# Kernel optimization log

Measured on AMD Instinct MI355X. Metric: run time of the kernel, lower is better.

Reference implementation:

```python
import jax, jax.numpy as jnp
import numpy as np
import math

H = 128          # num_heads
DN = 128         # qk_nope_head_dim
DR = 64          # qk_rope_head_dim
DV = 128         # v_head_dim
RQ = 1536        # q_lora_rank
RKV = 512        # kv_lora_rank
HSZ = 5120       # hidden_size
EPS = 1e-6


def rms_norm(x, w, eps=EPS):
    var = jnp.mean(x * x, axis=-1, keepdims=True)
    return x * jax.lax.rsqrt(var + eps) * w


def rope(x):
    # x: [b, h, s, d] ; standard NeoX-style rotary, base 10000, positions 0..s-1
    d = x.shape[-1]
    s = x.shape[-2]
    inv_freq = 1.0 / (10000.0 ** (jnp.arange(0, d, 2, dtype=jnp.float32) / d))  # [d/2]
    t = jnp.arange(s, dtype=jnp.float32)
    freqs = jnp.outer(t, inv_freq)                      # [s, d/2]
    cos = jnp.concatenate([jnp.cos(freqs)] * 2, -1)     # [s, d]
    sin = jnp.concatenate([jnp.sin(freqs)] * 2, -1)
    x1, x2 = jnp.split(x, 2, axis=-1)
    rot = jnp.concatenate([-x2, x1], axis=-1)
    return (x * cos + rot * sin).astype(x.dtype)


def setup_inputs() -> dict:
    key = jax.random.key(0)
    ks = jax.random.split(key, 8)
    std = 0.02
    hidden_states = jax.random.normal(ks[0], (1, 1024, HSZ), dtype=jnp.float32)
    # weights stored [in, out] (transposed vs torch nn.Linear)
    Wq_c = jax.random.normal(ks[1], (HSZ, RQ), dtype=jnp.float32) * std
    q_norm_w = jnp.ones((RQ,), dtype=jnp.float32)
    Wq_d = jax.random.normal(ks[2], (RQ, H * (DN + DR)), dtype=jnp.float32) * std
    Wkv_c = jax.random.normal(ks[3], (HSZ, RKV + DR), dtype=jnp.float32) * std
    kv_norm_w = jnp.ones((RKV,), dtype=jnp.float32)
    Wkv_d = jax.random.normal(ks[4], (RKV, H * (DN + DV)), dtype=jnp.float32) * std
    Wo = jax.random.normal(ks[5], (H * DV, HSZ), dtype=jnp.float32) * std
    return {"hidden_states": hidden_states, "Wq_c": Wq_c, "q_norm_w": q_norm_w,
            "Wq_d": Wq_d, "Wkv_c": Wkv_c, "kv_norm_w": kv_norm_w,
            "Wkv_d": Wkv_d, "Wo": Wo}


def reference(hidden_states, Wq_c, q_norm_w, Wq_d, Wkv_c, kv_norm_w, Wkv_d, Wo):
    B, S, _ = hidden_states.shape
    # --- Query: compress -> RMSNorm -> decompress ---
    q = rms_norm(hidden_states @ Wq_c, q_norm_w) @ Wq_d          # [B,S,H*(DN+DR)]
    q = q.reshape(B, S, H, DN + DR).transpose(0, 2, 1, 3)        # [B,H,S,DN+DR]
    q_nope, q_rope = q[..., :DN], q[..., DN:]
    # --- KV: compress (this is the compressed_kv_cache) ---
    compress_kv_full = hidden_states @ Wkv_c                     # [B,S,RKV+DR]
    compressed_kv_cache = jax.lax.stop_gradient(compress_kv_full)
    compress_kv = compress_kv_full[..., :RKV]
    k_rope = compress_kv_full[..., RKV:][:, None, :, :]          # [B,1,S,DR]
    # --- KV decompress ---
    kv = rms_norm(compress_kv, kv_norm_w) @ Wkv_d                # [B,S,H*(DN+DV)]
    kv = kv.reshape(B, S, H, DN + DV).transpose(0, 2, 1, 3)      # [B,H,S,DN+DV]
    k_nope, v = kv[..., :DN], kv[..., DN:]
    # --- split RoPE on rope slices only ---
    q_rope = rope(q_rope)                                        # [B,H,S,DR]
    k_rope = rope(k_rope)                                        # [B,1,S,DR]
    # --- concat nope|rope (k_rope broadcasts over heads) ---
    qc = jnp.concatenate([q_nope, q_rope], axis=-1)              # [B,H,S,DN+DR]
    kc = jnp.concatenate([k_nope, jnp.broadcast_to(k_rope, (B, H, S, DR))], axis=-1)
    # --- attention ---
    scale = 1.0 / math.sqrt(DN + DR)
    scores = jnp.einsum('bhqd,bhkd->bhqk', qc, kc) * scale       # [B,H,S,S]
    probs = jax.nn.softmax(scores.astype(jnp.float32), axis=-1).astype(qc.dtype)
    out = jnp.einsum('bhqk,bhkd->bhqd', probs, v)                # [B,H,S,DV]
    out = out.transpose(0, 2, 1, 3).reshape(B, S, H * DV)
    out = out @ Wo                                               # [B,S,HSZ]
    return out, compressed_kv_cache
```

## Files before the change

### kernel.cpp

```cpp
#include <hip/hip_runtime.h>


typedef __attribute__((ext_vector_type(8))) short short8;
typedef __attribute__((ext_vector_type(4))) float f32x4;
typedef unsigned short u16;

__device__ __forceinline__ u16 f2bf(float f) {
  union { float f; unsigned u; } v; v.f = f;
  unsigned r = v.u + 0x7fffu + ((v.u >> 16) & 1u);
  return (u16)(r >> 16);
}
__device__ __forceinline__ float bf2f(u16 s) {
  union { unsigned u; float f; } v; v.u = ((unsigned)s) << 16; return v.f;
}

__device__ __forceinline__ void gl_lds16(const u16* g, u16* l) {
  __builtin_amdgcn_global_load_lds(
      (const __attribute__((address_space(1))) void*)g,
      (__attribute__((address_space(3))) void*)l,
      16, 0, 0);
}

#define BARX()  asm volatile("s_barrier" ::: "memory")
#define LGKM0() do { asm volatile("s_waitcnt lgkmcnt(0)" ::: "memory"); \
                     __builtin_amdgcn_sched_barrier(0); } while (0)
#define VMW(n)  asm volatile("s_waitcnt vmcnt(" #n ")" ::: "memory")

__global__ void k_zero(float* __restrict__ p, int n4) {
  int i = blockIdx.x * 256 + threadIdx.x;
  if (i < n4) ((float4*)p)[i] = make_float4(0.f, 0.f, 0.f, 0.f);
}

__global__ void k_cast(const float* __restrict__ in, u16* __restrict__ out, int n4) {
  int i = blockIdx.x * 256 + threadIdx.x;
  if (i < n4) {
    float4 v = ((const float4*)in)[i];
    ushort4 o;
    o.x = f2bf(v.x); o.y = f2bf(v.y); o.z = f2bf(v.z); o.w = f2bf(v.w);
    ((ushort4*)out)[i] = o;
  }
}

__global__ void k_wt(const float* __restrict__ W, u16* __restrict__ WT,
                     int K, int N) {
  __shared__ u16 t[32][33];
  int n0 = blockIdx.x * 32, k0 = blockIdx.y * 32;
  int tx = threadIdx.x, ty = threadIdx.y;
#pragma unroll
  for (int r = 0; r < 4; r++) {
    int kl = ty + r * 8, n = n0 + tx;
    float v = (n < N) ? W[(size_t)(k0 + kl) * N + n] : 0.f;
    t[kl][tx] = f2bf(v);
  }
  __syncthreads();
#pragma unroll
  for (int r = 0; r < 4; r++) {
    int nl = ty + r * 8;
    WT[(size_t)(n0 + nl) * K + k0 + tx] = t[tx][nl];
  }
}

template<int OUT_MODE>
__global__ __launch_bounds__(256) void k_gemm_bt(
    const u16* __restrict__ A, const u16* __restrict__ BT,
    void* __restrict__ Cv, int M, int N, int K, int kChunk)
{
  __shared__ u16 As[128 * 32];
  __shared__ u16 Bs[128 * 32];
  const int tid = threadIdx.x;
  const int wave = tid >> 6, lane = tid & 63;
  const int qd = lane >> 4, l = lane & 15;
  const int bn0 = blockIdx.x * 128, bm0 = blockIdx.y * 128;
  const int k0 = blockIdx.z * kChunk;
  const int wrow = (wave >> 1) * 64, wcol = (wave & 1) * 64;
  const f32x4 fzero = {0.f, 0.f, 0.f, 0.f};

  f32x4 acc[4][4];
#pragma unroll
  for (int i = 0; i < 4; i++)
#pragma unroll
    for (int j = 0; j < 4; j++) acc[i][j] = fzero;

  const int sm = wave * 16 + (lane >> 2);
  const int sc = (lane & 3) * 8;
  const u16* a0 = A  + (size_t)(bm0 + sm) * K + sc;
  const u16* a1 = A  + (size_t)(bm0 + 64 + sm) * K + sc;
  const u16* b0 = BT + (size_t)(bn0 + sm) * K + sc;
  const u16* b1 = BT + (size_t)(bn0 + 64 + sm) * K + sc;
  u16* aD0 = As + wave * 512;
  u16* aD1 = As + 2048 + wave * 512;
  u16* bD0 = Bs + wave * 512;
  u16* bD1 = Bs + 2048 + wave * 512;

  const int kEnd = k0 + kChunk;
  for (int kt = k0; kt < kEnd; kt += 32) {
    gl_lds16(a0 + kt, aD0);
    gl_lds16(a1 + kt, aD1);
    gl_lds16(b0 + kt, bD0);
    gl_lds16(b1 + kt, bD1);
    __syncthreads();

    short8 af[4], bfr[4];
#pragma unroll
    for (int i = 0; i < 4; i++) af[i]  = *(const short8*)&As[(wrow + i * 16 + l) * 32 + qd * 8];
#pragma unroll
    for (int j = 0; j < 4; j++) bfr[j] = *(const short8*)&Bs[(wcol + j * 16 + l) * 32 + qd * 8];
#pragma unroll
    for (int i = 0; i < 4; i++)
#pragma unroll
      for (int j = 0; j < 4; j++)
        acc[i][j] = __builtin_amdgcn_mfma_f32_16x16x32_bf16(af[i], bfr[j], acc[i][j], 0, 0, 0);
    __syncthreads();
  }

#pragma unroll
  for (int i = 0; i < 4; i++) {
    int r = bm0 + wrow + i * 16 + qd * 4;
#pragma unroll
    for (int j = 0; j < 4; j++) {
      int c = bn0 + wcol + j * 16 + l;
      if (c < N) {
#pragma unroll
        for (int reg = 0; reg < 4; ++reg) {
          if (OUT_MODE == 1)
            ((u16*)Cv)[(size_t)(r + reg) * N + c] = f2bf(acc[i][j][reg]);
          else if (OUT_MODE == 0)
            ((float*)Cv)[(size_t)(r + reg) * N + c] = acc[i][j][reg];
          else
            atomicAdd(&((float*)Cv)[(size_t)(r + reg) * N + c], acc[i][j][reg]);
        }
      }
    }
  }
}

template<int OUT_MODE>
__global__ __launch_bounds__(512, 2) void k_gemm256(
    const u16* __restrict__ A, const u16* __restrict__ BT, void* __restrict__ Cv,
    int M, int N, int K, int kChunk)
{
  __shared__ u16 As[2][16384];
  __shared__ u16 Bs[2][16384];
  const int tid = threadIdx.x;
  const int w = tid >> 6, lane = tid & 63;
  const int wm = w >> 2, wn = w & 3;
  const int qd = lane >> 4, l = lane & 15;

  const int gx = gridDim.x, gy = gridDim.y;
  const int nwg = gx * gy * gridDim.z;
  int lin = blockIdx.x + gx * (blockIdx.y + gy * blockIdx.z);
  int lin2 = (lin & 7) * (nwg >> 3) + (lin >> 3);
  const int bx = lin2 % gx;
  const int byz = lin2 / gx;
  const int bm0 = (byz % gy) * 256;
  const int bn0 = bx * 256;
  const int k0  = (byz / gy) * kChunk;
  const int kcap = K - k0;
  const int myChunk = (kcap < kChunk) ? kcap : kChunk;
  const int ntiles = myChunk >> 6;
  const int niter  = ntiles >> 1;

  f32x4 acc[8][4];
  const f32x4 fz = {0.f, 0.f, 0.f, 0.f};
#pragma unroll
  for (int i = 0; i < 8; i++)
#pragma unroll
    for (int j = 0; j < 4; j++) acc[i][j] = fz;

#define STG(matP, rb, tI, hf, dstB)                                           \
  {                                                                           \
    const int _kt = k0 + (tI) * 64;                                           \
    _Pragma("unroll")                                                         \
    for (int _L = 0; _L < 2; ++_L) {                                          \
      const int _ob = (hf) * 8192 + _L * 4096 + w * 512;    \
      const int _o  = _ob + lane * 8;                                         \
      const int _r  = _o >> 6;                                                \
      const int _c  = (_o & 63) ^ ((_r & 7) << 3);                            \
      gl_lds16((matP) + (size_t)((rb) + _r) * K + _kt + _c, (dstB) + _ob);    \
    }                                                                         \
  }

#define LDA4(buf, mh)                                                         \
  _Pragma("unroll")                                                           \
  for (int _i = 0; _i < 4; ++_i) {                                            \
    const int _row = wm * 128 + (mh) * 64 + _i * 16 + l;                      \
    const int _sw = (_row & 7) << 3;                                          \
    af[_i][0] = *(const short8*)&(buf)[_row * 64 + ((qd * 8) ^ _sw)];         \
    af[_i][1] = *(const short8*)&(buf)[_row * 64 + ((32 + qd * 8) ^ _sw)];    \
  }

#define LDB2(buf, nh, dst)                                                    \
  _Pragma("unroll")                                                           \
  for (int _j = 0; _j < 2; ++_j) {                                            \
    const int _row = wn * 64 + (nh) * 32 + _j * 16 + l;                       \
    const int _sw = (_row & 7) << 3;                                          \
    dst[_j][0] = *(const short8*)&(buf)[_row * 64 + ((qd * 8) ^ _sw)];        \
    dst[_j][1] = *(const short8*)&(buf)[_row * 64 + ((32 + qd * 8) ^ _sw)];   \
  }

#define MFQ(mh, nh, bsrc)                                                     \
  __builtin_amdgcn_s_setprio(1);                                              \
  _Pragma("unroll")                                                           \
  for (int _i = 0; _i < 4; ++_i)                                              \
    _Pragma("unroll")                                                         \
    for (int _j = 0; _j < 2; ++_j) {                                          \
      f32x4 _a = acc[(mh) * 4 + _i][(nh) * 2 + _j];                           \
      _a = __builtin_amdgcn_mfma_f32_16x16x32_bf16(af[_i][0], bsrc[_j][0], _a, 0, 0, 0); \
      _a = __builtin_amdgcn_mfma_f32_16x16x32_bf16(af[_i][1], bsrc[_j][1], _a, 0, 0, 0); \
      acc[(mh) * 4 + _i][(nh) * 2 + _j] = _a;                                 \
    }                                                                         \
  __builtin_amdgcn_s_setprio(0);

  STG(BT, bn0, 0, 0, Bs[0]); STG(BT, bn0, 0, 1, Bs[0]);
  STG(A,  bm0, 0, 0, As[0]); STG(A,  bm0, 0, 1, As[0]);
  STG(BT, bn0, 1, 0, Bs[1]); STG(BT, bn0, 1, 1, Bs[1]);
  STG(A,  bm0, 1, 0, As[1]);
  VMW(6);
  BARX();

  short8 af[4][2], bf0[2][2], bf1[2][2];
  for (int j = 0; j < niter; ++j) {
    int t2 = 2 * j + 2; if (t2 >= ntiles) t2 -= ntiles;
    int t3 = t2 + 1;

    LDA4(As[0], 0); LDB2(Bs[0], 0, bf0);
    STG(A, bm0, 2 * j + 1, 1, As[1]);
    BARX(); LGKM0();
    MFQ(0, 0, bf0);
    BARX();

    LDB2(Bs[0], 1, bf1);
    BARX(); LGKM0();
    MFQ(0, 1, bf1);
    BARX();

    LDA4(As[0], 1);
    STG(BT, bn0, t2, 0, Bs[0]); STG(BT, bn0, t2, 1, Bs[0]);
    BARX(); LGKM0();
    MFQ(1, 1, bf1);
    BARX();

    STG(A, bm0, t2, 0, As[0]);
    VMW(6);
    BARX(); LGKM0();
    MFQ(1, 0, bf0);
    BARX();

    LDA4(As[1], 0); LDB2(Bs[1], 0, bf0);
    STG(A, bm0, t2, 1, As[0]);
    BARX(); LGKM0();
    MFQ(0, 0, bf0);
    BARX();

    LDB2(Bs[1], 1, bf1);
    BARX(); LGKM0();
    MFQ(0, 1, bf1);
    BARX();

    LDA4(As[1], 1);
    STG(BT, bn0, t3, 0, Bs[1]); STG(BT, bn0, t3, 1, Bs[1]);
    BARX(); LGKM0();
    MFQ(1, 1, bf1);
    BARX();

    STG(A, bm0, t3, 0, As[1]);
    VMW(6);
    BARX(); LGKM0();
    MFQ(1, 0, bf0);
    BARX();
  }
  asm volatile("s_waitcnt vmcnt(0)" ::: "memory");

#undef STG
#undef LDA4
#undef LDB2
#undef MFQ

#pragma unroll
  for (int i = 0; i < 8; ++i) {
    int r = bm0 + wm * 128 + i * 16 + qd * 4;
#pragma unroll
    for (int jj = 0; jj < 4; ++jj) {
      int c = bn0 + wn * 64 + jj * 16 + l;
#pragma unroll
      for (int reg = 0; reg < 4; ++reg) {
        if (OUT_MODE == 1)
          ((u16*)Cv)[(size_t)(r + reg) * N + c] = f2bf(acc[i][jj][reg]);
        else
          atomicAdd(&((float*)Cv)[(size_t)(r + reg) * N + c], acc[i][jj][reg]);
      }
    }
  }
}

__global__ void k_rmsnorm(const float* __restrict__ in, int istride, int W,
                          const float* __restrict__ w, u16* __restrict__ out) {
  int row = blockIdx.x, tid = threadIdx.x;
  const float* x = in + (size_t)row * istride;
  float s = 0.f;
  for (int i = tid; i < W; i += 256) { float v = x[i]; s += v * v; }
#pragma unroll
  for (int o = 32; o; o >>= 1) s += __shfl_xor(s, o);
  __shared__ float red[4];
  if ((tid & 63) == 0) red[tid >> 6] = s;
  __syncthreads();
  float tot = red[0] + red[1] + red[2] + red[3];
  float sc = rsqrtf(tot / (float)W + 1e-6f);
  for (int i = tid; i < W; i += 256)
    out[(size_t)row * W + i] = f2bf(x[i] * sc * w[i]);
}

__global__ void k_rope_q(u16* __restrict__ q) {
  int idx = blockIdx.x * 256 + threadIdx.x;
  int s = idx >> 12, r = idx & 4095, h = r >> 5, i = r & 31;
  float inv = expf((float)i * (-logf(10000.f) / 32.f));
  float ang = (float)s * inv, sn, cs;
  sincosf(ang, &sn, &cs);
  u16* p1 = q + (size_t)s * 24576 + h * 192 + 128 + i;
  u16* p2 = p1 + 32;
  float x1 = bf2f(*p1), x2 = bf2f(*p2);
  *p1 = f2bf(x1 * cs - x2 * sn);
  *p2 = f2bf(x2 * cs + x1 * sn);
}

__global__ void k_rope_k(const float* __restrict__ ckv, u16* __restrict__ kr) {
  int idx = blockIdx.x * 256 + threadIdx.x;
  int s = idx >> 5, i = idx & 31;
  float inv = expf((float)i * (-logf(10000.f) / 32.f));
  float ang = (float)s * inv, sn, cs;
  sincosf(ang, &sn, &cs);
  const float* src = ckv + (size_t)s * 576 + 512;
  float x1 = src[i], x2 = src[i + 32];
  kr[s * 64 + i]      = f2bf(x1 * cs - x2 * sn);
  kr[s * 64 + 32 + i] = f2bf(x2 * cs + x1 * sn);
}

__global__ void k_transpose_v(const u16* __restrict__ kv, u16* __restrict__ vt) {
  __shared__ u16 tile[32][33];
  int h = blockIdx.z, s0 = blockIdx.x * 32, d0 = blockIdx.y * 32;
  int tx = threadIdx.x, ty = threadIdx.y;
#pragma unroll
  for (int k2 = 0; k2 < 4; k2++) {
    int r = ty + k2 * 8;
    tile[r][tx] = kv[(size_t)(s0 + r) * 32768 + h * 256 + 128 + d0 + tx];
  }
  __syncthreads();
#pragma unroll
  for (int k2 = 0; k2 < 4; k2++) {
    int r = ty + k2 * 8;
    vt[(size_t)h * 131072 + (size_t)(d0 + r) * 1024 + s0 + tx] = tile[tx][r];
  }
}

__global__ __launch_bounds__(256, 2) void k_attn(
    const u16* __restrict__ q,
    const u16* __restrict__ kvn,
    const u16* __restrict__ kr,
    const u16* __restrict__ vt,
    u16* __restrict__ o)
{
  __shared__ u16 Ks[64][200];
  __shared__ u16 Vs[128][72];
  __shared__ u16 Ps[4][16][64];
  const int h = blockIdx.x, q0 = blockIdx.y * 64;
  const int tid = threadIdx.x, wave = tid >> 6, lane = tid & 63;
  const int qd = lane >> 4, l = lane & 15;
  const float scale = 0.07216878364870323f;
  const f32x4 fzero = {0.f, 0.f, 0.f, 0.f};

  short8 qf[6];
  {
    const u16* qp = q + (size_t)(q0 + wave * 16 + l) * 24576 + h * 192 + qd * 8;
#pragma unroll
    for (int kk = 0; kk < 6; kk++) qf[kk] = *(const short8*)(qp + kk * 32);
  }

  f32x4 Of[8];
#pragma unroll
  for (int jt = 0; jt < 8; jt++) Of[jt] = fzero;
  float m_i[4] = {-1e30f, -1e30f, -1e30f, -1e30f};
  float l_i[4] = {0.f, 0.f, 0.f, 0.f};

  for (int kt = 0; kt < 16; ++kt) {
    const int kv0 = kt * 64;
    __syncthreads();
#pragma unroll
    for (int it = 0; it < 6; ++it) {
      int ci = it * 256 + tid;
      int r = ci / 24, c = ci % 24;
      int col0 = c * 8;
      const u16* src = (col0 < 128)
          ? kvn + (size_t)(kv0 + r) * 32768 + h * 256 + col0
          : kr + (size_t)(kv0 + r) * 64 + (col0 - 128);
      *(short8*)&Ks[r][col0] = *(const short8*)src;
    }
#pragma unroll
    for (int it = 0; it < 4; ++it) {
      int ci = it * 256 + tid;
      int dv = ci >> 3, c = ci & 7;
      *(short8*)&Vs[dv][c * 8] =
          *(const short8*)(vt + (size_t)h * 131072 + (size_t)dv * 1024 + kv0 + c * 8);
    }
    __syncthreads();

    f32x4 sf[4];
#pragma unroll
    for (int j = 0; j < 4; j++) sf[j] = fzero;
#pragma unroll
    for (int kk = 0; kk < 6; kk++)
#pragma unroll
      for (int j = 0; j < 4; j++) {
        short8 bf = *(const short8*)&Ks[j * 16 + l][kk * 32 + qd * 8];
        sf[j] = __builtin_amdgcn_mfma_f32_16x16x32_bf16(qf[kk], bf, sf[j], 0, 0, 0);
      }
#pragma unroll
    for (int j = 0; j < 4; j++) sf[j] *= scale;

#pragma unroll
    for (int reg = 0; reg < 4; ++reg) {
      float mx = fmaxf(fmaxf(sf[0][reg], sf[1][reg]), fmaxf(sf[2][reg], sf[3][reg]));
#pragma unroll
      for (int off = 1; off < 16; off <<= 1) mx = fmaxf(mx, __shfl_xor(mx, off));
      float mnew = fmaxf(m_i[reg], mx);
      float alpha = expf(m_i[reg] - mnew);
      m_i[reg] = mnew;
      float rs = 0.f;
      int prow = qd * 4 + reg;
#pragma unroll
      for (int j = 0; j < 4; j++) {
        float p = expf(sf[j][reg] - mnew);
        rs += p;
        int g = (j * 2 + (l >> 3)) ^ (prow & 7);
        Ps[wave][prow][g * 8 + (l & 7)] = f2bf(p);
      }
#pragma unroll
      for (int off = 1; off < 16; off <<= 1) rs += __shfl_xor(rs, off);
      l_i[reg] = l_i[reg] * alpha + rs;
#pragma unroll
      for (int jt = 0; jt < 8; jt++) Of[jt][reg] *= alpha;
    }

#pragma unroll
    for (int ks = 0; ks < 2; ++ks) {
      short8 pf = *(const short8*)&Ps[wave][l][(((ks * 4 + qd) ^ (l & 7))) * 8];
#pragma unroll
      for (int jt = 0; jt < 8; jt++) {
        short8 vf = *(const short8*)&Vs[jt * 16 + l][ks * 32 + qd * 8];
        Of[jt] = __builtin_amdgcn_mfma_f32_16x16x32_bf16(pf, vf, Of[jt], 0, 0, 0);
      }
    }
  }

#pragma unroll
  for (int reg = 0; reg < 4; ++reg) {
    float inv_l = 1.f / l_i[reg];
    int row = q0 + wave * 16 + qd * 4 + reg;
#pragma unroll
    for (int jt = 0; jt < 8; jt++)
      o[(size_t)row * 16384 + h * 128 + jt * 16 + l] = f2bf(Of[jt][reg] * inv_l);
  }
}

extern "C" void kernel_launch(void* const* d_in, const int* in_sizes, int n_in,
                              void* d_out, int out_size, void* d_ws, size_t ws_size,
                              hipStream_t stream)
{
  const float* hidden = (const float*)d_in[0];
  const float* Wq_c   = (const float*)d_in[1];
  const float* q_nw   = (const float*)d_in[2];
  const float* Wq_d   = (const float*)d_in[3];
  const float* Wkv_c  = (const float*)d_in[4];
  const float* kv_nw  = (const float*)d_in[5];
  const float* Wkv_d  = (const float*)d_in[6];
  const float* Wo     = (const float*)d_in[7];

  float* out = (float*)d_out;
  float* ckv = out + (size_t)1024 * 5120;

  char* ws = (char*)d_ws;
  u16*   h_bf  = (u16*)ws;   ws += (size_t)1024 * 5120 * 2;
  float* q_c   = (float*)ws; ws += (size_t)1024 * 1536 * 4;
  u16*   q_n   = (u16*)ws;   ws += (size_t)1024 * 1536 * 2;
  u16*   qbuf  = (u16*)ws;   ws += (size_t)1024 * 24576 * 2;
  u16*   kv_n  = (u16*)ws;   ws += (size_t)1024 * 512 * 2;
  u16*   kvbuf = (u16*)ws;   ws += (size_t)1024 * 32768 * 2;
  u16*   krope = (u16*)ws;   ws += (size_t)1024 * 64 * 2;
  u16*   vt    = (u16*)ws;   ws += (size_t)128 * 128 * 1024 * 2;
  u16*   attno = (u16*)ws;   ws += (size_t)1024 * 16384 * 2;
  u16*   wtqc  = (u16*)ws;   ws += (size_t)1536 * 5120 * 2;
  u16*   wtkvc = (u16*)ws;   ws += (size_t)640 * 5120 * 2;
  u16*   wtqd  = (u16*)ws;   ws += (size_t)24576 * 1536 * 2;
  u16*   wtkvd = (u16*)ws;   ws += (size_t)32768 * 512 * 2;
  u16*   wto   = (u16*)ws;   ws += (size_t)5120 * 16384 * 2;

  dim3 b256(256), b512(512), bwt(32, 8);

  k_zero<<<5696, b256, 0, stream>>>(out, (1024 * 5120 + 1024 * 576) / 4);
  k_zero<<<1536, b256, 0, stream>>>(q_c, 1024 * 1536 / 4);

  k_wt<<<dim3(48, 160),  bwt, 0, stream>>>(Wq_c,  wtqc,  5120, 1536);
  k_wt<<<dim3(20, 160),  bwt, 0, stream>>>(Wkv_c, wtkvc, 5120, 576);
  k_wt<<<dim3(768, 48),  bwt, 0, stream>>>(Wq_d,  wtqd,  1536, 24576);
  k_wt<<<dim3(1024, 16), bwt, 0, stream>>>(Wkv_d, wtkvd, 512,  32768);
  k_wt<<<dim3(160, 512), bwt, 0, stream>>>(Wo,    wto,   16384, 5120);

  k_cast<<<5120, b256, 0, stream>>>(hidden, h_bf, 1024 * 5120 / 4);

  k_gemm_bt<2><<<dim3(12, 8, 4), b256, 0, stream>>>(h_bf, wtqc,  q_c, 1024, 1536, 5120, 1280);
  k_gemm_bt<2><<<dim3(5, 8, 8),  b256, 0, stream>>>(h_bf, wtkvc, ckv, 1024, 576,  5120, 640);

  k_rmsnorm<<<1024, b256, 0, stream>>>(q_c, 1536, 1536, q_nw, q_n);
  k_rmsnorm<<<1024, b256, 0, stream>>>(ckv, 576,  512,  kv_nw, kv_n);

  k_gemm256<1><<<dim3(96, 4, 1),  b512, 0, stream>>>(q_n,  wtqd,  qbuf,  1024, 24576, 1536, 1536);
  k_gemm256<1><<<dim3(128, 4, 1), b512, 0, stream>>>(kv_n, wtkvd, kvbuf, 1024, 32768, 512,  512);

  k_rope_q<<<16384, b256, 0, stream>>>(qbuf);
  k_rope_k<<<128,   b256, 0, stream>>>(ckv, krope);

  k_transpose_v<<<dim3(32, 4, 128), dim3(32, 8), 0, stream>>>(kvbuf, vt);

  k_attn<<<dim3(128, 16), b256, 0, stream>>>(qbuf, kvbuf, krope, vt, attno);

  k_gemm256<2><<<dim3(20, 4, 3), b512, 0, stream>>>(attno, wto, out, 1024, 5120, 16384, 5504);
}
```

Baseline: 1.543 ms.

## Transpose attention MFMA operands, keep P in registers via bpermute, stage output

```diff
diff --git a/kernel.cpp b/kernel.cpp
--- a/kernel.cpp
+++ b/kernel.cpp
@@ -12,6 +12,9 @@
 }
 __device__ __forceinline__ float bf2f(u16 s) {
   union { unsigned u; float f; } v; v.u = ((unsigned)s) << 16; return v.f;
+}
+__device__ __forceinline__ unsigned pk2(float a, float b) {
+  return (unsigned)f2bf(a) | ((unsigned)f2bf(b) << 16);
 }
 
 __device__ __forceinline__ void gl_lds16(const u16* g, u16* l) {
@@ -352,7 +355,7 @@
   }
 }
 
-__global__ __launch_bounds__(256, 2) void k_attn(
+__global__ __launch_bounds__(256, 3) void k_attn(
     const u16* __restrict__ q,
     const u16* __restrict__ kvn,
     const u16* __restrict__ kr,
@@ -361,10 +364,12 @@
 {
   __shared__ u16 Ks[64][200];
   __shared__ u16 Vs[128][72];
-  __shared__ u16 Ps[4][16][64];
   const int h = blockIdx.x, q0 = blockIdx.y * 64;
   const int tid = threadIdx.x, wave = tid >> 6, lane = tid & 63;
   const int qd = lane >> 4, l = lane & 15;
+  const bool hi5 = lane >= 32;
+  const int bidx0 = (l + ((lane >> 4) & 1) * 32) << 2;
+  const int bidx1 = bidx0 + 64;
   const float scale = 0.07216878364870323f;
   const f32x4 fzero = {0.f, 0.f, 0.f, 0.f};
 
@@ -378,8 +383,8 @@
   f32x4 Of[8];
 #pragma unroll
   for (int jt = 0; jt < 8; jt++) Of[jt] = fzero;
-  float m_i[4] = {-1e30f, -1e30f, -1e30f, -1e30f};
-  float l_i[4] = {0.f, 0.f, 0.f, 0.f};
+  float m_i = -1e30f;
+  float l_i = 0.f;
 
   for (int kt = 0; kt < 16; ++kt) {
     const int kv0 = kt * 64;
@@ -406,58 +411,93 @@
     f32x4 sf[4];
 #pragma unroll
     for (int j = 0; j < 4; j++) sf[j] = fzero;
+    __builtin_amdgcn_s_setprio(1);
 #pragma unroll
     for (int kk = 0; kk < 6; kk++)
 #pragma unroll
       for (int j = 0; j < 4; j++) {
-        short8 bf = *(const short8*)&Ks[j * 16 + l][kk * 32 + qd * 8];
-        sf[j] = __builtin_amdgcn_mfma_f32_16x16x32_bf16(qf[kk], bf, sf[j], 0, 0, 0);
+        short8 kf = *(const short8*)&Ks[j * 16 + l][kk * 32 + qd * 8];
+        sf[j] = __builtin_amdgcn_mfma_f32_16x16x32_bf16(kf, qf[kk], sf[j], 0, 0, 0);
       }
+    __builtin_amdgcn_s_setprio(0);
 #pragma unroll
     for (int j = 0; j < 4; j++) sf[j] *= scale;
 
-#pragma unroll
-    for (int reg = 0; reg < 4; ++reg) {
-      float mx = fmaxf(fmaxf(sf[0][reg], sf[1][reg]), fmaxf(sf[2][reg], sf[3][reg]));
-#pragma unroll
-      for (int off = 1; off < 16; off <<= 1) mx = fmaxf(mx, __shfl_xor(mx, off));
-      float mnew = fmaxf(m_i[reg], mx);
-      float alpha = expf(m_i[reg] - mnew);
-      m_i[reg] = mnew;
-      float rs = 0.f;
-      int prow = qd * 4 + reg;
-#pragma unroll
-      for (int j = 0; j < 4; j++) {
-        float p = expf(sf[j][reg] - mnew);
+    float mx0 = fmaxf(fmaxf(sf[0][0], sf[0][1]), fmaxf(sf[0][2], sf[0][3]));
+    float mx1 = fmaxf(fmaxf(sf[1][0], sf[1][1]), fmaxf(sf[1][2], sf[1][3]));
+    float mx2 = fmaxf(fmaxf(sf[2][0], sf[2][1]), fmaxf(sf[2][2], sf[2][3]));
+    float mx3 = fmaxf(fmaxf(sf[3][0], sf[3][1]), fmaxf(sf[3][2], sf[3][3]));
+    float mx = fmaxf(fmaxf(mx0, mx1), fmaxf(mx2, mx3));
+    mx = fmaxf(mx, __shfl_xor(mx, 16));
+    mx = fmaxf(mx, __shfl_xor(mx, 32));
+    float mnew = fmaxf(m_i, mx);
+    float alpha = expf(m_i - mnew);
+    m_i = mnew;
+
+    float rs = 0.f;
+#pragma unroll
+    for (int j = 0; j < 4; j++)
+#pragma unroll
+      for (int r = 0; r < 4; r++) {
+        float p = expf(sf[j][r] - mnew);
+        sf[j][r] = p;
         rs += p;
-        int g = (j * 2 + (l >> 3)) ^ (prow & 7);
-        Ps[wave][prow][g * 8 + (l & 7)] = f2bf(p);
       }
-#pragma unroll
-      for (int off = 1; off < 16; off <<= 1) rs += __shfl_xor(rs, off);
-      l_i[reg] = l_i[reg] * alpha + rs;
-#pragma unroll
-      for (int jt = 0; jt < 8; jt++) Of[jt][reg] *= alpha;
+    rs += __shfl_xor(rs, 16);
+    rs += __shfl_xor(rs, 32);
+    l_i = l_i * alpha + rs;
+#pragma unroll
+    for (int jt = 0; jt < 8; jt++) Of[jt] *= alpha;
+
+    unsigned cv[4][2];
+#pragma unroll
+    for (int j = 0; j < 4; j++) {
+      cv[j][0] = pk2(sf[j][0], sf[j][1]);
+      cv[j][1] = pk2(sf[j][2], sf[j][3]);
     }
 
 #pragma unroll
     for (int ks = 0; ks < 2; ++ks) {
-      short8 pf = *(const short8*)&Ps[wave][l][(((ks * 4 + qd) ^ (l & 7))) * 8];
+      union { unsigned u[4]; short8 v; } pfu;
+#pragma unroll
+      for (int t1 = 0; t1 < 2; ++t1) {
+        const int bidx = t1 ? bidx1 : bidx0;
+#pragma unroll
+        for (int t0 = 0; t0 < 2; ++t0) {
+          int pa = __builtin_amdgcn_ds_bpermute(bidx, (int)cv[2 * ks][t0]);
+          int pb = __builtin_amdgcn_ds_bpermute(bidx, (int)cv[2 * ks + 1][t0]);
+          pfu.u[t1 * 2 + t0] = (unsigned)(hi5 ? pb : pa);
+        }
+      }
+      __builtin_amdgcn_s_setprio(1);
 #pragma unroll
       for (int jt = 0; jt < 8; jt++) {
         short8 vf = *(const short8*)&Vs[jt * 16 + l][ks * 32 + qd * 8];
-        Of[jt] = __builtin_amdgcn_mfma_f32_16x16x32_bf16(pf, vf, Of[jt], 0, 0, 0);
+        Of[jt] = __builtin_amdgcn_mfma_f32_16x16x32_bf16(vf, pfu.v, Of[jt], 0, 0, 0);
       }
-    }
-  }
-
-#pragma unroll
-  for (int reg = 0; reg < 4; ++reg) {
-    float inv_l = 1.f / l_i[reg];
-    int row = q0 + wave * 16 + qd * 4 + reg;
-#pragma unroll
-    for (int jt = 0; jt < 8; jt++)
-      o[(size_t)row * 16384 + h * 128 + jt * 16 + l] = f2bf(Of[jt][reg] * inv_l);
+      __builtin_amdgcn_s_setprio(0);
+    }
+  }
+
+  __syncthreads();
+  float inv_l = 1.f / l_i;
+  u16* Ot = ((u16*)Ks) + wave * 2048;
+#pragma unroll
+  for (int jt = 0; jt < 8; jt++)
+#pragma unroll
+    for (int reg = 0; reg < 4; ++reg) {
+      int slot = jt * 2 + (qd >> 1);
+      int off  = (qd & 1) * 4 + reg;
+      int ps   = (slot & 8) | ((slot & 7) ^ (l & 7));
+      Ot[l * 128 + ps * 8 + off] = f2bf(Of[jt][reg] * inv_l);
+    }
+#pragma unroll
+  for (int it = 0; it < 4; ++it) {
+    int idx = it * 64 + lane;
+    int qq = idx >> 4, g = idx & 15;
+    int ps = (g & 8) | ((g & 7) ^ (qq & 7));
+    short8 v = *(const short8*)&Ot[qq * 128 + ps * 8];
+    *(short8*)&o[(size_t)(q0 + wave * 16 + qq) * 16384 + h * 128 + g * 8] = v;
   }
 }
 
```

Result: no change. 1.525 ms (-1.2%).
